# Kernel tuning notes

Hardware: AMD Instinct MI355X
Metric: run time of the kernel (lower is better)

The kernel has to match this reference:

```python
import jax, jax.numpy as jnp
import numpy as np
from jax import lax

B, D, H, W = 8, 256, 56, 56
DH = 32            # d_head
HEADS = D // DH    # 8
WIN = 7            # window size
TOPK = 8           # top-k windows
DM = 4 * D         # mlp hidden = 1024
EPS = 1e-5


def bn(x, g, b, m, v):
    # inference-mode BatchNorm2d over channel dim of NCHW
    return g[:, None, None] * (x - m[:, None, None]) * lax.rsqrt(v[:, None, None] + EPS) + b[:, None, None]


def conv1x1(x, w):
    return jnp.einsum('bchw,oc->bohw', x, w)


def setup_inputs() -> dict:
    key = jax.random.key(0)
    ks = jax.random.split(key, 24)
    s = 0.05
    return {
        'x': jax.random.normal(ks[0], (B, D, H, W), jnp.float32),
        'g1': jax.random.uniform(ks[1], (D,)) + 0.5,
        'b1': jax.random.normal(ks[2], (D,)) * s,
        'm1': jax.random.normal(ks[3], (D,)) * s,
        'v1': jax.random.uniform(ks[4], (D,)) + 0.5,
        'W_qkv': jax.random.normal(ks[5], (3 * D, D)) * s,
        'W_merge': jax.random.normal(ks[6], (D, D)) * s,
        'b_merge': jax.random.normal(ks[7], (D,)) * s,
        'W1': jax.random.normal(ks[8], (DM, D)) * s,
        'g2': jax.random.uniform(ks[9], (DM,)) + 0.5,
        'b2': jax.random.normal(ks[10], (DM,)) * s,
        'm2': jax.random.normal(ks[11], (DM,)) * s,
        'v2': jax.random.uniform(ks[12], (DM,)) + 0.5,
        'Wdw': jax.random.normal(ks[13], (DM, 1, 3, 3)) * s,
        'g3': jax.random.uniform(ks[14], (DM,)) + 0.5,
        'b3': jax.random.normal(ks[15], (DM,)) * s,
        'm3': jax.random.normal(ks[16], (DM,)) * s,
        'v3': jax.random.uniform(ks[17], (DM,)) + 0.5,
        'W2': jax.random.normal(ks[18], (D, DM)) * s,
        'g4': jax.random.uniform(ks[19], (D,)) + 0.5,
        'b4': jax.random.normal(ks[20], (D,)) * s,
        'm4': jax.random.normal(ks[21], (D,)) * s,
        'v4': jax.random.uniform(ks[22], (D,)) + 0.5,
    }


def _forward(x, g1, b1, m1, v1, W_qkv, W_merge, b_merge,
             W1, g2, b2, m2, v2, Wdw, g3, b3, m3, v3, W2, g4, b4, m4, v4):
    b_, d, Hh, Ww = x.shape
    nh, nw = Hh // WIN, Ww // WIN
    nWnd, ww = nh * nw, WIN * WIN

    # qkv projection: BN -> GELU -> 1x1 conv
    h = jax.nn.gelu(bn(x, g1, b1, m1, v1), approximate=False)
    qkv = conv1x1(h, W_qkv)
    q, k, v = jnp.split(qkv, 3, axis=1)  # each [b, d, H, W]

    def part(t):  # -> [b, heads, nWnd, ww, dh]
        t = t.reshape(b_, HEADS, DH, nh, WIN, nw, WIN)
        return jnp.transpose(t, (0, 1, 3, 5, 4, 6, 2)).reshape(b_, HEADS, nWnd, ww, DH)

    qw, kw, vw = part(q), part(k), part(v)

    # window-level routing: mean-pooled q/k per window, top-k window selection
    def pool(t):  # [b, d, H, W] -> [b, nWnd, d]
        t = t.reshape(b_, d, nh, WIN, nw, WIN).mean(axis=(3, 5))
        return t.reshape(b_, d, nWnd).transpose(0, 2, 1)

    qr, kr = pool(q), pool(k)
    aff = jnp.einsum('bnd,bmd->bnm', qr, kr)        # [b, nWnd, nWnd]
    idx = lax.top_k(aff, TOPK)[1]                    # [b, nWnd, TOPK]

    def gath(t, i):  # t [heads, nWnd, ww, dh], i [nWnd, TOPK]
        return t[:, i]  # [heads, nWnd, TOPK, ww, dh]

    kg = jax.vmap(gath)(kw, idx).reshape(b_, HEADS, nWnd, TOPK * ww, DH)
    vg = jax.vmap(gath)(vw, idx).reshape(b_, HEADS, nWnd, TOPK * ww, DH)

    scores = jnp.einsum('bhnqd,bhnkd->bhnqk', qw, kg) / jnp.sqrt(jnp.float32(DH))
    attn = jax.nn.softmax(scores, axis=-1)
    out = jnp.einsum('bhnqk,bhnkd->bhnqd', attn, vg)  # [b, heads, nWnd, ww, dh]

    # un-partition back to [b, d, H, W]
    out = out.reshape(b_, HEADS, nh, nw, WIN, WIN, DH)
    msg = jnp.transpose(out, (0, 1, 6, 2, 4, 3, 5)).reshape(b_, d, Hh, Ww)

    # merge (1x1 conv with bias) + residual
    x = x + conv1x1(msg, W_merge) + b_merge[None, :, None, None]

    # MB mlp block: 1x1 -> BN -> GELU -> dw3x3 -> BN -> GELU -> 1x1 -> BN
    h2 = conv1x1(x, W1)
    h2 = jax.nn.gelu(bn(h2, g2, b2, m2, v2), approximate=False)
    h2 = lax.conv_general_dilated(h2, Wdw, (1, 1), 'SAME',
                                  feature_group_count=DM,
                                  dimension_numbers=('NCHW', 'OIHW', 'NCHW'))
    h2 = jax.nn.gelu(bn(h2, g3, b3, m3, v3), approximate=False)
    h2 = conv1x1(h2, W2)
    h2 = bn(h2, g4, b4, m4, v4)
    return x + h2


def reference(x, g1, b1, m1, v1, W_qkv, W_merge, b_merge,
              W1, g2, b2, m2, v2, Wdw, g3, b3, m3, v3, W2, g4, b4, m4, v4):
    return _forward(x, g1, b1, m1, v1, W_qkv, W_merge, b_merge,
                    W1, g2, b2, m2, v2, Wdw, g3, b3, m3, v3, W2, g4, b4, m4, v4)
```

## Files before the change

kernel.cpp:

```cpp
#include <hip/hip_runtime.h>
#include <cstdint>
#include <cstddef>

#define BB 8
#define PP 3136
#define EPSV 1e-5f
#define SCQK 0.17677669529663687f

using bf16x8 = __attribute__((ext_vector_type(8))) short;
using f32x4  = __attribute__((ext_vector_type(4))) float;

__device__ __forceinline__ float bf2f(unsigned short u) {
    union { float f; unsigned int i; } c; c.i = ((unsigned int)u) << 16; return c.f;
}
__device__ __forceinline__ unsigned short f2bf(float f) {
    union { float f; unsigned int i; } c; c.f = f;
    unsigned int r = c.i + 0x7FFFu + ((c.i >> 16) & 1u);
    return (unsigned short)(r >> 16);
}
__device__ __forceinline__ float gelu_f(float t) {
    return 0.5f * t * (1.0f + erff(t * 0.70710678118654752440f));
}
__device__ __forceinline__ float gelu_fast(float x) {
    float z = 1.5957691216057308f * (x + 0.044715f * x * x * x);
    return x / (1.0f + __expf(-z));
}
__device__ __forceinline__ void async16(const void* g, void* s) {
    __builtin_amdgcn_global_load_lds(
        (const __attribute__((address_space(1))) unsigned int*)g,
        (__attribute__((address_space(3))) unsigned int*)s, 16, 0, 0);
}
__device__ __forceinline__ uint4 pack8(const float* v) {
    uint4 o;
    o.x = (unsigned)f2bf(v[0]) | ((unsigned)f2bf(v[1]) << 16);
    o.y = (unsigned)f2bf(v[2]) | ((unsigned)f2bf(v[3]) << 16);
    o.z = (unsigned)f2bf(v[4]) | ((unsigned)f2bf(v[5]) << 16);
    o.w = (unsigned)f2bf(v[6]) | ((unsigned)f2bf(v[7]) << 16);
    return o;
}

__global__ __launch_bounds__(256) void cvt_all_k(
    const float* __restrict__ Wq, const float* __restrict__ Wm,
    const float* __restrict__ W1, const float* __restrict__ W2,
    unsigned short* __restrict__ dq, unsigned short* __restrict__ dm,
    unsigned short* __restrict__ d1, unsigned short* __restrict__ d2)
{
    int i = blockIdx.x * 256 + threadIdx.x;
    if (i < 196608) dq[i] = f2bf(Wq[i]);
    else if (i < 262144) dm[i - 196608] = f2bf(Wm[i - 196608]);
    else if (i < 524288) d1[i - 262144] = f2bf(W1[i - 262144]);
    else d2[i - 524288] = f2bf(W2[i - 524288]);
}

__global__ __launch_bounds__(256) void transin_k(const float* __restrict__ x,
    const float* __restrict__ g1, const float* __restrict__ b1,
    const float* __restrict__ m1, const float* __restrict__ v1,
    float* __restrict__ x_pm, unsigned short* __restrict__ h_bf)
{
    __shared__ float tile[64][65];
    __shared__ float gam[64], bet[64], mu[64], rst[64];
    const int p0 = blockIdx.x * 64, c0 = blockIdx.y * 64, b = blockIdx.z;
    const int t = threadIdx.x;
    if (t < 64) { int c = c0 + t; gam[t] = g1[c]; bet[t] = b1[c]; mu[t] = m1[c]; rst[t] = rsqrtf(v1[c] + EPSV); }
    {
        int cl = t >> 2, px = (t & 3) * 16;
        const float* src = x + ((size_t)(b * 256 + c0 + cl)) * PP + p0 + px;
        #pragma unroll
        for (int i4 = 0; i4 < 4; i4++) {
            float4 r0 = *(const float4*)(src + i4 * 4);
            tile[cl][px + i4*4 + 0] = r0.x; tile[cl][px + i4*4 + 1] = r0.y;
            tile[cl][px + i4*4 + 2] = r0.z; tile[cl][px + i4*4 + 3] = r0.w;
        }
    }
    __syncthreads();
    {
        int pl = t >> 2, cb = (t & 3) * 16;
        float raw[16], hg[16];
        #pragma unroll
        for (int i = 0; i < 16; i++) {
            float vv = tile[cb + i][pl];
            raw[i] = vv;
            hg[i] = gelu_fast(gam[cb + i] * (vv - mu[cb + i]) * rst[cb + i] + bet[cb + i]);
        }
        size_t off = ((size_t)b * PP + p0 + pl) * 256 + c0 + cb;
        float* xd = x_pm + off;
        #pragma unroll
        for (int i4 = 0; i4 < 4; i4++) {
            float4 o; o.x = raw[i4*4]; o.y = raw[i4*4+1]; o.z = raw[i4*4+2]; o.w = raw[i4*4+3];
            *(float4*)(xd + i4 * 4) = o;
        }
        uint4* hd = (uint4*)(h_bf + off);
        hd[0] = pack8(&hg[0]);
        hd[1] = pack8(&hg[8]);
    }
}

template<int EPI>
__global__ __launch_bounds__(256) void gemm_mfma_k(
    const unsigned short* __restrict__ Aact,
    const unsigned short* __restrict__ Wbf,
    const int K, const int Mout,
    void* __restrict__ C1, void* __restrict__ C2,
    const float* __restrict__ e0, const float* __restrict__ e1,
    const float* __restrict__ e2, const float* __restrict__ e3,
    const float* __restrict__ resid)
{
    __shared__ __align__(16) char smem[34816];
    unsigned short* As0 = (unsigned short*)smem;
    unsigned short* Bs0 = (unsigned short*)(smem + 16384);
    float* T = (float*)smem;

    const int tid = threadIdx.x;
    const int w = tid >> 6, lane = tid & 63, g = lane >> 4, l15 = lane & 15;
    const int wm = w >> 1, wn = w & 1;
    const size_t row0 = (size_t)blockIdx.x * 128;
    const int n0 = blockIdx.y * 128;
    const int srow = tid >> 2, scb = tid & 3;

    const f32x4 vzero = {0.f, 0.f, 0.f, 0.f};
    f32x4 acc[4][4];
    #pragma unroll
    for (int mf = 0; mf < 4; mf++)
        #pragma unroll
        for (int nf = 0; nf < 4; nf++) acc[mf][nf] = vzero;

    const int NT = K >> 5;

    auto STAGE = [&](int s) {
        const int k0 = s << 5;
        unsigned short* Ad = As0 + (s & 1) * 4096;
        unsigned short* Bd = Bs0 + (s & 1) * 4096;
        #pragma unroll
        for (int r = 0; r < 2; r++) {
            int row = r * 64 + srow;
            int cbp = scb ^ ((row >> 1) & 3);
            async16(Aact + (row0 + row) * K + k0 + cbp * 8, Ad + r * 2048 + w * 512);
            async16(Wbf + (size_t)(n0 + row) * K + k0 + cbp * 8, Bd + r * 2048 + w * 512);
        }
    };
    auto COMPUTE = [&](int t) {
        const unsigned short* Ab = As0 + (t & 1) * 4096;
        const unsigned short* Bb = Bs0 + (t & 1) * 4096;
        bf16x8 af[4], bfr[4];
        #pragma unroll
        for (int mf = 0; mf < 4; mf++) {
            int row = wm * 64 + mf * 16 + l15;
            int gb = g ^ ((row >> 1) & 3);
            af[mf] = *(const bf16x8*)&Ab[row * 32 + gb * 8];
        }
        #pragma unroll
        for (int nf = 0; nf < 4; nf++) {
            int row = wn * 64 + nf * 16 + l15;
            int gb = g ^ ((row >> 1) & 3);
            bfr[nf] = *(const bf16x8*)&Bb[row * 32 + gb * 8];
        }
        #pragma unroll
        for (int mf = 0; mf < 4; mf++)
            #pragma unroll
            for (int nf = 0; nf < 4; nf++)
                acc[mf][nf] = __builtin_amdgcn_mfma_f32_16x16x32_bf16(af[mf], bfr[nf], acc[mf][nf], 0, 0, 0);
    };

    STAGE(0);
    for (int t = 0; t < NT; ++t) {
        __syncthreads();
        if (t + 1 < NT) STAGE(t + 1);
        COMPUTE(t);
    }

    __syncthreads();
    const int erow = tid >> 1;
    const int ec0 = (tid & 1) * 32;
    #pragma unroll
    for (int pass = 0; pass < 2; ++pass) {
        if (pass) __syncthreads();
        if (wn == pass) {
            #pragma unroll
            for (int mf = 0; mf < 4; mf++)
                #pragma unroll
                for (int nf = 0; nf < 4; nf++)
                    #pragma unroll
                    for (int r = 0; r < 4; r++)
                        T[(wm * 64 + mf * 16 + g * 4 + r) * 68 + nf * 16 + l15] = acc[mf][nf][r];
        }
        __syncthreads();
        float vals[32];
        #pragma unroll
        for (int i = 0; i < 8; i++) {
            float4 v = *(const float4*)&T[erow * 68 + ec0 + i * 4];
            vals[i*4+0] = v.x; vals[i*4+1] = v.y; vals[i*4+2] = v.z; vals[i*4+3] = v.w;
        }
        const size_t prow = row0 + erow;
        const int mc0 = n0 + pass * 64 + ec0;
        const size_t off = prow * Mout + mc0;
        if (EPI == 0) {
            const float s = (mc0 < 256) ? SCQK : 1.0f;
            #pragma unroll
            for (int j = 0; j < 32; j++) vals[j] *= s;
            uint4* dst = (uint4*)((unsigned short*)C1 + off);
            #pragma unroll
            for (int i = 0; i < 4; i++) dst[i] = pack8(&vals[i * 8]);
        } else if (EPI == 1) {
            #pragma unroll
            for (int i = 0; i < 8; i++) {
                float4 bi = *(const float4*)(e0 + mc0 + i * 4);
                float4 rr = *(const float4*)(resid + off + i * 4);
                vals[i*4+0] += bi.x + rr.x; vals[i*4+1] += bi.y + rr.y;
                vals[i*4+2] += bi.z + rr.z; vals[i*4+3] += bi.w + rr.w;
            }
            float4* d1 = (float4*)((float*)C1 + off);
            #pragma unroll
            for (int i = 0; i < 8; i++) {
                float4 o; o.x = vals[i*4]; o.y = vals[i*4+1]; o.z = vals[i*4+2]; o.w = vals[i*4+3];
                d1[i] = o;
            }
            uint4* d2 = (uint4*)((unsigned short*)C2 + off);
            #pragma unroll
            for (int i = 0; i < 4; i++) d2[i] = pack8(&vals[i * 8]);
        } else if (EPI == 2) {
            #pragma unroll
            for (int i = 0; i < 8; i++) {
                float4 ga = *(const float4*)(e0 + mc0 + i * 4);
                float4 be = *(const float4*)(e1 + mc0 + i * 4);
                float4 mm = *(const float4*)(e2 + mc0 + i * 4);
                float4 vv = *(const float4*)(e3 + mc0 + i * 4);
                vals[i*4+0] = gelu_fast(ga.x * (vals[i*4+0] - mm.x) * rsqrtf(vv.x + EPSV) + be.x);
                vals[i*4+1] = gelu_fast(ga.y * (vals[i*4+1] - mm.y) * rsqrtf(vv.y + EPSV) + be.y);
                vals[i*4+2] = gelu_fast(ga.z * (vals[i*4+2] - mm.z) * rsqrtf(vv.z + EPSV) + be.z);
                vals[i*4+3] = gelu_fast(ga.w * (vals[i*4+3] - mm.w) * rsqrtf(vv.w + EPSV) + be.w);
            }
            uint4* dst = (uint4*)((unsigned short*)C1 + off);
            #pragma unroll
            for (int i = 0; i < 4; i++) dst[i] = pack8(&vals[i * 8]);
        } else {
            #pragma unroll
            for (int i = 0; i < 8; i++) {
                float4 ga = *(const float4*)(e0 + mc0 + i * 4);
                float4 be = *(const float4*)(e1 + mc0 + i * 4);
                float4 mm = *(const float4*)(e2 + mc0 + i * 4);
                float4 vv = *(const float4*)(e3 + mc0 + i * 4);
                float4 rr = *(const float4*)(resid + off + i * 4);
                vals[i*4+0] = ga.x * (vals[i*4+0] - mm.x) * rsqrtf(vv.x + EPSV) + be.x + rr.x;
                vals[i*4+1] = ga.y * (vals[i*4+1] - mm.y) * rsqrtf(vv.y + EPSV) + be.y + rr.y;
                vals[i*4+2] = ga.z * (vals[i*4+2] - mm.z) * rsqrtf(vv.z + EPSV) + be.z + rr.z;
                vals[i*4+3] = ga.w * (vals[i*4+3] - mm.w) * rsqrtf(vv.w + EPSV) + be.w + rr.w;
            }
            float4* d1 = (float4*)((float*)C1 + off);
            #pragma unroll
            for (int i = 0; i < 8; i++) {
                float4 o; o.x = vals[i*4]; o.y = vals[i*4+1]; o.z = vals[i*4+2]; o.w = vals[i*4+3];
                d1[i] = o;
            }
        }
    }
}

__global__ __launch_bounds__(256) void poolh_k(const float* __restrict__ x_pm,
    const float* __restrict__ g1, const float* __restrict__ b1,
    const float* __restrict__ m1, const float* __restrict__ v1,
    float* __restrict__ ph)
{
    __shared__ float part[4][256];
    __shared__ float gam[256], bet[256], mu[256], rst[256];
    const int n = blockIdx.x, b = blockIdx.y, t = threadIdx.x;
    gam[t] = g1[t]; bet[t] = b1[t]; mu[t] = m1[t]; rst[t] = rsqrtf(v1[t] + EPSV);
    __syncthreads();
    const int c4 = (t & 63) * 4, pg = t >> 6;
    float s0 = 0.f, s1 = 0.f, s2 = 0.f, s3 = 0.f;
    for (int j = pg; j < 49; j += 4) {
        int p = ((n >> 3) * 7 + j / 7) * 56 + (n & 7) * 7 + j % 7;
        float4 vx = *(const float4*)(x_pm + ((size_t)b * PP + p) * 256 + c4);
        s0 += gelu_f(gam[c4+0] * (vx.x - mu[c4+0]) * rst[c4+0] + bet[c4+0]);
        s1 += gelu_f(gam[c4+1] * (vx.y - mu[c4+1]) * rst[c4+1] + bet[c4+1]);
        s2 += gelu_f(gam[c4+2] * (vx.z - mu[c4+2]) * rst[c4+2] + bet[c4+2]);
        s3 += gelu_f(gam[c4+3] * (vx.w - mu[c4+3]) * rst[c4+3] + bet[c4+3]);
    }
    part[pg][c4 + 0] = s0; part[pg][c4 + 1] = s1; part[pg][c4 + 2] = s2; part[pg][c4 + 3] = s3;
    __syncthreads();
    float tot = part[0][t] + part[1][t] + part[2][t] + part[3][t];
    ph[((size_t)b * 64 + n) * 256 + t] = tot * (1.0f / 49.0f);
}

__global__ __launch_bounds__(256) void qrkr_k(const float* __restrict__ ph,
    const float* __restrict__ Wqkv, float* __restrict__ qr, float* __restrict__ kr)
{
    __shared__ float row[256];
    const int n = blockIdx.x, b = blockIdx.y, t = threadIdx.x;
    row[t] = ph[((size_t)b * 64 + n) * 256 + t];
    __syncthreads();
    const float* wq = Wqkv + (size_t)t * 256;
    const float* wk = Wqkv + (size_t)(256 + t) * 256;
    float aq = 0.f, ak = 0.f;
    #pragma unroll 4
    for (int k = 0; k < 256; k += 4) {
        float4 a4 = *(const float4*)(wq + k);
        float4 b4 = *(const float4*)(wk + k);
        aq += row[k]*a4.x + row[k+1]*a4.y + row[k+2]*a4.z + row[k+3]*a4.w;
        ak += row[k]*b4.x + row[k+1]*b4.y + row[k+2]*b4.z + row[k+3]*b4.w;
    }
    qr[((size_t)b * 64 + n) * 256 + t] = aq;
    kr[((size_t)b * 64 + n) * 256 + t] = ak;
}

__global__ __launch_bounds__(64) void topk_k(const float* __restrict__ qr,
    const float* __restrict__ kr, int* __restrict__ idxb)
{
    const int n = blockIdx.x, b_ = blockIdx.y;
    const int tid = threadIdx.x;
    __shared__ float qrow[256];
    *reinterpret_cast<float4*>(&qrow[tid * 4]) =
        *reinterpret_cast<const float4*>(qr + ((size_t)(b_ * 64) + n) * 256 + tid * 4);
    __syncthreads();
    const float* kp = kr + ((size_t)(b_ * 64) + tid) * 256;
    float av = 0.f;
    #pragma unroll 4
    for (int c = 0; c < 256; c++) av = fmaf(qrow[c], kp[c], av);
    for (int t = 0; t < 8; t++) {
        float v = av; int id = tid;
        #pragma unroll
        for (int off = 32; off; off >>= 1) {
            float v2 = __shfl_xor(v, off);
            int id2 = __shfl_xor(id, off);
            if (v2 > v || (v2 == v && id2 < id)) { v = v2; id = id2; }
        }
        if (tid == 0) idxb[((b_ * 64) + n) * 8 + t] = id;
        if (tid == id) av = -1e30f;
    }
}

__global__ __launch_bounds__(256) void attn_mfma_k(const unsigned short* __restrict__ qkv,
    const int* __restrict__ idxb, unsigned short* __restrict__ msg)
{
    __shared__ __align__(16) unsigned short Ks[64 * 40];
    __shared__ __align__(16) unsigned short Vt[32 * 72];
    __shared__ __align__(16) unsigned short Pr[4][16 * 72];
    const int n = blockIdx.x, h = blockIdx.y, b = blockIdx.z;
    const int tid = threadIdx.x;
    const int w = tid >> 6, lane = tid & 63, g = lane >> 4, l15 = lane & 15;

    for (int e = tid; e < 64 * 40; e += 256) Ks[e] = 0;
    for (int e = tid; e < 32 * 72; e += 256) Vt[e] = 0;

    const int iq = w * 16 + l15;
    bf16x8 qf = {0, 0, 0, 0, 0, 0, 0, 0};
    if (iq < 49) {
        int p = ((n >> 3) * 7 + iq / 7) * 56 + (n & 7) * 7 + iq % 7;
        qf = *(const bf16x8*)(qkv + ((size_t)b * PP + p) * 768 + h * 32 + g * 8);
    }
    const f32x4 vzero = {0.f, 0.f, 0.f, 0.f};
    f32x4 o0 = vzero, o1 = vzero;
    float mrow = -1e30f, lrow = 0.f;

    const bool act = tid < 196;
    const int jrow = tid >> 2, c8 = (tid & 3) * 8;
    uint4 kk_r = {0,0,0,0}, vv_r = {0,0,0,0};
    auto LOADW = [&](int t) {
        int wsrc = idxb[((b * 64) + n) * 8 + t];
        int p = ((wsrc >> 3) * 7 + jrow / 7) * 56 + (wsrc & 7) * 7 + jrow % 7;
        const unsigned short* srcp = qkv + ((size_t)b * PP + p) * 768 + 256 + h * 32 + c8;
        kk_r = *(const uint4*)srcp;
        vv_r = *(const uint4*)(srcp + 256);
    };
    if (act) LOADW(0);

    for (int t = 0; t < 8; t++) {
        __syncthreads();
        if (act) {
            *(uint4*)&Ks[jrow * 40 + c8] = kk_r;
            const unsigned short* pv = (const unsigned short*)&vv_r;
            #pragma unroll
            for (int jj = 0; jj < 8; jj++) {
                int dh = c8 + jj;
                Vt[dh * 72 + (jrow ^ (((dh >> 3) & 3) << 3))] = pv[jj];
            }
            if (t < 7) LOADW(t + 1);
        }
        __syncthreads();
        f32x4 s[4];
        #pragma unroll
        for (int nf = 0; nf < 4; nf++) {
            bf16x8 kf = *(const bf16x8*)&Ks[(nf * 16 + l15) * 40 + g * 8];
            s[nf] = __builtin_amdgcn_mfma_f32_16x16x32_bf16(kf, qf, vzero, 0, 0, 0);
        }
        float sv[16];
        #pragma unroll
        for (int nf = 0; nf < 4; nf++)
            #pragma unroll
            for (int r = 0; r < 4; r++) {
                int j = nf * 16 + g * 4 + r;
                sv[nf * 4 + r] = (j < 49) ? s[nf][r] : -1e30f;
            }
        float wmx = sv[0];
        #pragma unroll
        for (int e = 1; e < 16; e++) wmx = fmaxf(wmx, sv[e]);
        wmx = fmaxf(wmx, __shfl_xor(wmx, 16));
        wmx = fmaxf(wmx, __shfl_xor(wmx, 32));
        float mn = fmaxf(mrow, wmx);
        float corr = __expf(mrow - mn);
        mrow = mn;
        float rsum = 0.f;
        #pragma unroll
        for (int e = 0; e < 16; e++) { float pe = __expf(sv[e] - mn); sv[e] = pe; rsum += pe; }
        rsum += __shfl_xor(rsum, 16);
        rsum += __shfl_xor(rsum, 32);
        lrow = lrow * corr + rsum;
        #pragma unroll
        for (int r = 0; r < 4; r++) { o0[r] *= corr; o1[r] *= corr; }
        #pragma unroll
        for (int nf = 0; nf < 4; nf++) {
            uint2 pw;
            pw.x = (unsigned)f2bf(sv[nf*4+0]) | ((unsigned)f2bf(sv[nf*4+1]) << 16);
            pw.y = (unsigned)f2bf(sv[nf*4+2]) | ((unsigned)f2bf(sv[nf*4+3]) << 16);
            *(uint2*)&Pr[w][l15 * 72 + nf * 16 + g * 4] = pw;
        }
        asm volatile("s_waitcnt lgkmcnt(0)" ::: "memory");
        #pragma unroll
        for (int ks = 0; ks < 2; ks++) {
            const int j0 = ks * 32 + g * 8;
            bf16x8 pf  = *(const bf16x8*)&Pr[w][l15 * 72 + j0];
            bf16x8 vf0 = *(const bf16x8*)&Vt[l15 * 72 + (j0 ^ (((l15 >> 3) & 1) << 3))];
            bf16x8 vf1 = *(const bf16x8*)&Vt[(16 + l15) * 72 + (j0 ^ ((2 + (l15 >> 3)) << 3))];
            o0 = __builtin_amdgcn_mfma_f32_16x16x32_bf16(vf0, pf, o0, 0, 0, 0);
            o1 = __builtin_amdgcn_mfma_f32_16x16x32_bf16(vf1, pf, o1, 0, 0, 0);
        }
    }
    if (iq < 49) {
        float inv = 1.0f / lrow;
        int p = ((n >> 3) * 7 + iq / 7) * 56 + (n & 7) * 7 + iq % 7;
        size_t off = ((size_t)b * PP + p) * 256 + h * 32;
        uint2 w0, w1;
        w0.x = (unsigned)f2bf(o0[0]*inv) | ((unsigned)f2bf(o0[1]*inv) << 16);
        w0.y = (unsigned)f2bf(o0[2]*inv) | ((unsigned)f2bf(o0[3]*inv) << 16);
        w1.x = (unsigned)f2bf(o1[0]*inv) | ((unsigned)f2bf(o1[1]*inv) << 16);
        w1.y = (unsigned)f2bf(o1[2]*inv) | ((unsigned)f2bf(o1[3]*inv) << 16);
        *(uint2*)(msg + off + g * 4) = w0;
        *(uint2*)(msg + off + 16 + g * 4) = w1;
    }
}

__global__ __launch_bounds__(256) void dwconv_k(const unsigned short* __restrict__ in,
    const float* __restrict__ w9,
    const float* __restrict__ g3, const float* __restrict__ b3,
    const float* __restrict__ m3, const float* __restrict__ v3,
    unsigned short* __restrict__ out)
{
    __shared__ __align__(16) unsigned short tl[100 * 64];
    const int sx = blockIdx.x % 7, sy = blockIdx.x / 7;
    const int c0 = blockIdx.y * 64, b = blockIdx.z;
    const int t = threadIdx.x;
    for (int e = t; e < 800; e += 256) {
        int pos = e >> 3, c8 = (e & 7) * 8;
        int iy = sy * 8 + pos / 10 - 1, ix = sx * 8 + pos % 10 - 1;
        uint4 val = {0u, 0u, 0u, 0u};
        if (iy >= 0 && iy < 56 && ix >= 0 && ix < 56)
            val = *(const uint4*)(in + ((size_t)b * PP + iy * 56 + ix) * 1024 + c0 + c8);
        *(uint4*)&tl[pos * 64 + c8] = val;
    }
    __syncthreads();
    const int c2 = (t & 31) * 2, pg = t >> 5;
    const int c = c0 + c2;
    float w0[9], w1[9];
    #pragma unroll
    for (int i = 0; i < 9; i++) { w0[i] = w9[c * 9 + i]; w1[i] = w9[(c + 1) * 9 + i]; }
    const float ga0 = g3[c], be0 = b3[c], mu0 = m3[c], rs0 = rsqrtf(v3[c] + EPSV);
    const float ga1 = g3[c+1], be1 = b3[c+1], mu1 = m3[c+1], rs1 = rsqrtf(v3[c+1] + EPSV);
    #pragma unroll
    for (int q = 0; q < 8; q++) {
        int pos = pg * 8 + q, y = pos >> 3, xq = pos & 7;
        float s0 = 0.f, s1 = 0.f;
        #pragma unroll
        for (int dy = 0; dy < 3; dy++)
            #pragma unroll
            for (int dx = 0; dx < 3; dx++) {
                unsigned int u = *(const unsigned int*)&tl[((y + dy) * 10 + xq + dx) * 64 + c2];
                s0 = fmaf(bf2f((unsigned short)(u & 0xffffu)), w0[dy * 3 + dx], s0);
                s1 = fmaf(bf2f((unsigned short)(u >> 16)), w1[dy * 3 + dx], s1);
            }
        float y0 = gelu_fast(ga0 * (s0 - mu0) * rs0 + be0);
        float y1 = gelu_fast(ga1 * (s1 - mu1) * rs1 + be1);
        unsigned int ow = (unsigned int)f2bf(y0) | ((unsigned int)f2bf(y1) << 16);
        size_t off = ((size_t)b * PP + (sy * 8 + y) * 56 + sx * 8 + xq) * 1024 + c;
        *(unsigned int*)&out[off] = ow;
    }
}

__global__ __launch_bounds__(256) void transout_k(const float* __restrict__ out_pm,
    float* __restrict__ dout)
{
    __shared__ float tile[64][65];
    const int p0 = blockIdx.x * 64, c0 = blockIdx.y * 64, b = blockIdx.z;
    const int t = threadIdx.x;
    {
        int pl = t >> 2, cx = (t & 3) * 16;
        const float* src = out_pm + ((size_t)b * PP + p0 + pl) * 256 + c0 + cx;
        #pragma unroll
        for (int i4 = 0; i4 < 4; i4++) {
            float4 vv = *(const float4*)(src + i4 * 4);
            tile[pl][cx + i4*4 + 0] = vv.x; tile[pl][cx + i4*4 + 1] = vv.y;
            tile[pl][cx + i4*4 + 2] = vv.z; tile[pl][cx + i4*4 + 3] = vv.w;
        }
    }
    __syncthreads();
    {
        int cl = t >> 2, px = (t & 3) * 16;
        float* dst = dout + ((size_t)(b * 256 + c0 + cl)) * PP + p0 + px;
        #pragma unroll
        for (int i4 = 0; i4 < 4; i4++) {
            float4 o;
            o.x = tile[px + i4*4 + 0][cl]; o.y = tile[px + i4*4 + 1][cl];
            o.z = tile[px + i4*4 + 2][cl]; o.w = tile[px + i4*4 + 3][cl];
            *(float4*)(dst + i4 * 4) = o;
        }
    }
}

extern "C" void kernel_launch(void* const* d_in, const int* in_sizes, int n_in,
                              void* d_out, int out_size, void* d_ws, size_t ws_size,
                              hipStream_t stream)
{
    const float* x      = (const float*)d_in[0];
    const float* g1     = (const float*)d_in[1];
    const float* b1     = (const float*)d_in[2];
    const float* m1     = (const float*)d_in[3];
    const float* v1     = (const float*)d_in[4];
    const float* Wqkv   = (const float*)d_in[5];
    const float* Wmerge = (const float*)d_in[6];
    const float* bmerge = (const float*)d_in[7];
    const float* W1     = (const float*)d_in[8];
    const float* g2     = (const float*)d_in[9];
    const float* b2     = (const float*)d_in[10];
    const float* m2     = (const float*)d_in[11];
    const float* v2     = (const float*)d_in[12];
    const float* Wdw    = (const float*)d_in[13];
    const float* g3     = (const float*)d_in[14];
    const float* b3     = (const float*)d_in[15];
    const float* m3     = (const float*)d_in[16];
    const float* v3     = (const float*)d_in[17];
    const float* W2     = (const float*)d_in[18];
    const float* g4     = (const float*)d_in[19];
    const float* b4     = (const float*)d_in[20];
    const float* m4     = (const float*)d_in[21];
    const float* v4     = (const float*)d_in[22];

    char* ws = (char*)d_ws;
    float*          x_pm   = (float*)(ws + 0);
    float*          x2_pm  = (float*)(ws + 25690112);
    unsigned short* x2_bf  = (unsigned short*)(ws + 51380224);
    unsigned short* qkv_pm = (unsigned short*)(ws + 64225280);
    unsigned short* msg_pm = (unsigned short*)(ws + 102760448);
    unsigned short* t1     = (unsigned short*)(ws + 115605504);
    unsigned short* h_bf   = t1;
    unsigned short* t2     = (unsigned short*)(ws + 166985728);
    float*          ph     = (float*)(ws + 218365952);
    float*          qr     = (float*)(ws + 218890240);
    float*          kr     = (float*)(ws + 219414528);
    int*            idxb   = (int*)(ws + 219938816);
    unsigned short* Wqkv_b = (unsigned short*)(ws + 219955200);
    unsigned short* Wmrg_b = (unsigned short*)(ws + 220348416);
    unsigned short* W1_b   = (unsigned short*)(ws + 220479488);
    unsigned short* W2_b   = (unsigned short*)(ws + 221003776);
    float*          out_pm = x_pm;
    if (ws_size < 221528064) return;

    cvt_all_k<<<3072, 256, 0, stream>>>(Wqkv, Wmerge, W1, W2, Wqkv_b, Wmrg_b, W1_b, W2_b);
    transin_k<<<dim3(49, 4, BB), 256, 0, stream>>>(x, g1, b1, m1, v1, x_pm, h_bf);
    gemm_mfma_k<0><<<dim3(196, 6), 256, 0, stream>>>(h_bf, Wqkv_b, 256, 768,
        qkv_pm, nullptr, nullptr, nullptr, nullptr, nullptr, nullptr);
    poolh_k<<<dim3(64, BB), 256, 0, stream>>>(x_pm, g1, b1, m1, v1, ph);
    qrkr_k<<<dim3(64, BB), 256, 0, stream>>>(ph, Wqkv, qr, kr);
    topk_k<<<dim3(64, BB), 64, 0, stream>>>(qr, kr, idxb);
    attn_mfma_k<<<dim3(64, 8, BB), 256, 0, stream>>>(qkv_pm, idxb, msg_pm);
    gemm_mfma_k<1><<<dim3(196, 2), 256, 0, stream>>>(msg_pm, Wmrg_b, 256, 256,
        x2_pm, x2_bf, bmerge, nullptr, nullptr, nullptr, x_pm);
    gemm_mfma_k<2><<<dim3(196, 8), 256, 0, stream>>>(x2_bf, W1_b, 256, 1024,
        t1, nullptr, g2, b2, m2, v2, nullptr);
    dwconv_k<<<dim3(49, 16, BB), 256, 0, stream>>>(t1, Wdw, g3, b3, m3, v3, t2);
    gemm_mfma_k<3><<<dim3(196, 2), 256, 0, stream>>>(t2, W2_b, 1024, 256,
        out_pm, nullptr, g4, b4, m4, v4, x2_pm);
    transout_k<<<dim3(49, 4, BB), 256, 0, stream>>>(out_pm, (float*)d_out);
}
```

Baseline: 340.9 us.

## Load attention keys directly into registers and reshape GEMM epilogue staging

The attention kernel no longer stages K through shared memory. Each lane loads its key fragments straight from global memory into registers, the window indices are prefetched into registers once, and a scheduling barrier is added before the PV MFMAs. The GEMM epilogue now writes accumulators to LDS in four 32-row by 128-column passes instead of two 128-by-64 passes, which shrinks shared memory to 32 KB and gives each thread 16 contiguous output columns. The f32-to-bf16 conversion also switches to the HIP intrinsic. In exchange, K loads are now redundant across waves (each wave reloads all 64 keys) and the epilogue needs more barriers.

```diff
diff --git a/kernel.cpp b/kernel.cpp
--- a/kernel.cpp
+++ b/kernel.cpp
@@ -1,4 +1,5 @@
 #include <hip/hip_runtime.h>
+#include <hip/hip_bf16.h>
 #include <cstdint>
 #include <cstddef>
 
@@ -14,9 +15,8 @@
     union { float f; unsigned int i; } c; c.i = ((unsigned int)u) << 16; return c.f;
 }
 __device__ __forceinline__ unsigned short f2bf(float f) {
-    union { float f; unsigned int i; } c; c.f = f;
-    unsigned int r = c.i + 0x7FFFu + ((c.i >> 16) & 1u);
-    return (unsigned short)(r >> 16);
+    __hip_bfloat16 h = __float2bfloat16(f);
+    union { __hip_bfloat16 h; unsigned short u; } c; c.h = h; return c.u;
 }
 __device__ __forceinline__ float gelu_f(float t) {
     return 0.5f * t * (1.0f + erff(t * 0.70710678118654752440f));
@@ -105,7 +105,7 @@
     const float* __restrict__ e2, const float* __restrict__ e3,
     const float* __restrict__ resid)
 {
-    __shared__ __align__(16) char smem[34816];
+    __shared__ __align__(16) char smem[32768];
     unsigned short* As0 = (unsigned short*)smem;
     unsigned short* Bs0 = (unsigned short*)(smem + 16384);
     float* T = (float*)smem;
@@ -169,40 +169,40 @@
     }
 
     __syncthreads();
-    const int erow = tid >> 1;
-    const int ec0 = (tid & 1) * 32;
+    const int r32 = tid >> 3;
+    const int col0 = (tid & 7) * 16;
     #pragma unroll
-    for (int pass = 0; pass < 2; ++pass) {
-        if (pass) __syncthreads();
-        if (wn == pass) {
-            #pragma unroll
-            for (int mf = 0; mf < 4; mf++)
+    for (int p = 0; p < 4; ++p) {
+        if (p) __syncthreads();
+        if (wm == (p >> 1)) {
+            const int mfb = (p & 1) * 2;
+            #pragma unroll
+            for (int mo = 0; mo < 2; mo++)
                 #pragma unroll
                 for (int nf = 0; nf < 4; nf++)
                     #pragma unroll
                     for (int r = 0; r < 4; r++)
-                        T[(wm * 64 + mf * 16 + g * 4 + r) * 68 + nf * 16 + l15] = acc[mf][nf][r];
+                        T[(mo * 16 + g * 4 + r) * 132 + wn * 64 + nf * 16 + l15] = acc[mfb + mo][nf][r];
         }
         __syncthreads();
-        float vals[32];
-        #pragma unroll
-        for (int i = 0; i < 8; i++) {
-            float4 v = *(const float4*)&T[erow * 68 + ec0 + i * 4];
+        float vals[16];
+        #pragma unroll
+        for (int i = 0; i < 4; i++) {
+            float4 v = *(const float4*)&T[r32 * 132 + col0 + i * 4];
             vals[i*4+0] = v.x; vals[i*4+1] = v.y; vals[i*4+2] = v.z; vals[i*4+3] = v.w;
         }
-        const size_t prow = row0 + erow;
-        const int mc0 = n0 + pass * 64 + ec0;
+        const size_t prow = row0 + p * 32 + r32;
+        const int mc0 = n0 + col0;
         const size_t off = prow * Mout + mc0;
         if (EPI == 0) {
             const float s = (mc0 < 256) ? SCQK : 1.0f;
             #pragma unroll
-            for (int j = 0; j < 32; j++) vals[j] *= s;
+            for (int j = 0; j < 16; j++) vals[j] *= s;
             uint4* dst = (uint4*)((unsigned short*)C1 + off);
-            #pragma unroll
-            for (int i = 0; i < 4; i++) dst[i] = pack8(&vals[i * 8]);
+            dst[0] = pack8(&vals[0]); dst[1] = pack8(&vals[8]);
         } else if (EPI == 1) {
             #pragma unroll
-            for (int i = 0; i < 8; i++) {
+            for (int i = 0; i < 4; i++) {
                 float4 bi = *(const float4*)(e0 + mc0 + i * 4);
                 float4 rr = *(const float4*)(resid + off + i * 4);
                 vals[i*4+0] += bi.x + rr.x; vals[i*4+1] += bi.y + rr.y;
@@ -210,16 +210,15 @@
             }
             float4* d1 = (float4*)((float*)C1 + off);
             #pragma unroll
-            for (int i = 0; i < 8; i++) {
+            for (int i = 0; i < 4; i++) {
                 float4 o; o.x = vals[i*4]; o.y = vals[i*4+1]; o.z = vals[i*4+2]; o.w = vals[i*4+3];
                 d1[i] = o;
             }
             uint4* d2 = (uint4*)((unsigned short*)C2 + off);
-            #pragma unroll
-            for (int i = 0; i < 4; i++) d2[i] = pack8(&vals[i * 8]);
+            d2[0] = pack8(&vals[0]); d2[1] = pack8(&vals[8]);
         } else if (EPI == 2) {
             #pragma unroll
-            for (int i = 0; i < 8; i++) {
+            for (int i = 0; i < 4; i++) {
                 float4 ga = *(const float4*)(e0 + mc0 + i * 4);
                 float4 be = *(const float4*)(e1 + mc0 + i * 4);
                 float4 mm = *(const float4*)(e2 + mc0 + i * 4);
@@ -230,11 +229,10 @@
                 vals[i*4+3] = gelu_fast(ga.w * (vals[i*4+3] - mm.w) * rsqrtf(vv.w + EPSV) + be.w);
             }
             uint4* dst = (uint4*)((unsigned short*)C1 + off);
-            #pragma unroll
-            for (int i = 0; i < 4; i++) dst[i] = pack8(&vals[i * 8]);
+            dst[0] = pack8(&vals[0]); dst[1] = pack8(&vals[8]);
         } else {
             #pragma unroll
-            for (int i = 0; i < 8; i++) {
+            for (int i = 0; i < 4; i++) {
                 float4 ga = *(const float4*)(e0 + mc0 + i * 4);
                 float4 be = *(const float4*)(e1 + mc0 + i * 4);
                 float4 mm = *(const float4*)(e2 + mc0 + i * 4);
@@ -247,7 +245,7 @@
             }
             float4* d1 = (float4*)((float*)C1 + off);
             #pragma unroll
-            for (int i = 0; i < 8; i++) {
+            for (int i = 0; i < 4; i++) {
                 float4 o; o.x = vals[i*4]; o.y = vals[i*4+1]; o.z = vals[i*4+2]; o.w = vals[i*4+3];
                 d1[i] = o;
             }
@@ -331,14 +329,12 @@
 __global__ __launch_bounds__(256) void attn_mfma_k(const unsigned short* __restrict__ qkv,
     const int* __restrict__ idxb, unsigned short* __restrict__ msg)
 {
-    __shared__ __align__(16) unsigned short Ks[64 * 40];
     __shared__ __align__(16) unsigned short Vt[32 * 72];
     __shared__ __align__(16) unsigned short Pr[4][16 * 72];
     const int n = blockIdx.x, h = blockIdx.y, b = blockIdx.z;
     const int tid = threadIdx.x;
     const int w = tid >> 6, lane = tid & 63, g = lane >> 4, l15 = lane & 15;
 
-    for (int e = tid; e < 64 * 40; e += 256) Ks[e] = 0;
     for (int e = tid; e < 32 * 72; e += 256) Vt[e] = 0;
 
     const int iq = w * 16 + l15;
@@ -347,41 +343,52 @@
         int p = ((n >> 3) * 7 + iq / 7) * 56 + (n & 7) * 7 + iq % 7;
         qf = *(const bf16x8*)(qkv + ((size_t)b * PP + p) * 768 + h * 32 + g * 8);
     }
+    int widx[8];
+    {
+        const int* ip = idxb + ((b * 64) + n) * 8;
+        #pragma unroll
+        for (int t = 0; t < 8; t++) widx[t] = ip[t];
+    }
     const f32x4 vzero = {0.f, 0.f, 0.f, 0.f};
     f32x4 o0 = vzero, o1 = vzero;
     float mrow = -1e30f, lrow = 0.f;
 
     const bool act = tid < 196;
     const int jrow = tid >> 2, c8 = (tid & 3) * 8;
-    uint4 kk_r = {0,0,0,0}, vv_r = {0,0,0,0};
-    auto LOADW = [&](int t) {
-        int wsrc = idxb[((b * 64) + n) * 8 + t];
+    uint4 vv_r = {0,0,0,0};
+    auto LOADV = [&](int t) {
+        int wsrc = widx[t];
         int p = ((wsrc >> 3) * 7 + jrow / 7) * 56 + (wsrc & 7) * 7 + jrow % 7;
-        const unsigned short* srcp = qkv + ((size_t)b * PP + p) * 768 + 256 + h * 32 + c8;
-        kk_r = *(const uint4*)srcp;
-        vv_r = *(const uint4*)(srcp + 256);
+        vv_r = *(const uint4*)(qkv + ((size_t)b * PP + p) * 768 + 512 + h * 32 + c8);
     };
-    if (act) LOADW(0);
+    if (act) LOADV(0);
 
     for (int t = 0; t < 8; t++) {
+        const int wsrc = widx[t];
+        const int sy0 = (wsrc >> 3) * 7, sx0 = (wsrc & 7) * 7;
+        bf16x8 kf[4];
+        #pragma unroll
+        for (int nf = 0; nf < 4; nf++) {
+            int j = nf * 16 + l15;
+            int jc = (j < 49) ? j : 0;
+            int p = (sy0 + jc / 7) * 56 + sx0 + jc % 7;
+            kf[nf] = *(const bf16x8*)(qkv + ((size_t)b * PP + p) * 768 + 256 + h * 32 + g * 8);
+        }
         __syncthreads();
         if (act) {
-            *(uint4*)&Ks[jrow * 40 + c8] = kk_r;
             const unsigned short* pv = (const unsigned short*)&vv_r;
             #pragma unroll
             for (int jj = 0; jj < 8; jj++) {
                 int dh = c8 + jj;
                 Vt[dh * 72 + (jrow ^ (((dh >> 3) & 3) << 3))] = pv[jj];
             }
-            if (t < 7) LOADW(t + 1);
+            if (t < 7) LOADV(t + 1);
         }
         __syncthreads();
         f32x4 s[4];
         #pragma unroll
-        for (int nf = 0; nf < 4; nf++) {
-            bf16x8 kf = *(const bf16x8*)&Ks[(nf * 16 + l15) * 40 + g * 8];
-            s[nf] = __builtin_amdgcn_mfma_f32_16x16x32_bf16(kf, qf, vzero, 0, 0, 0);
-        }
+        for (int nf = 0; nf < 4; nf++)
+            s[nf] = __builtin_amdgcn_mfma_f32_16x16x32_bf16(kf[nf], qf, vzero, 0, 0, 0);
         float sv[16];
         #pragma unroll
         for (int nf = 0; nf < 4; nf++)
@@ -414,6 +421,7 @@
             *(uint2*)&Pr[w][l15 * 72 + nf * 16 + g * 4] = pw;
         }
         asm volatile("s_waitcnt lgkmcnt(0)" ::: "memory");
+        __builtin_amdgcn_sched_barrier(0);
         #pragma unroll
         for (int ks = 0; ks < 2; ks++) {
             const int j0 = ks * 32 + g * 8;
```

Measured after the change: 336.5 us. About the same (-1.3%).
